# Kernel tuning notes

Hardware: AMD Instinct MI355X
Metric: run time of the kernel (lower is better)

The kernel has to match this reference:

```python
import jax, jax.numpy as jnp
import numpy as np

H = 12       # num heads
D = 64       # head dim
EPS = 1e-5

def rms_norm(x, eps=EPS):
    var = jnp.mean(jnp.square(x), axis=-1, keepdims=True)
    return x * jax.lax.rsqrt(var + eps)

def rotate_half(x):
    x1, x2 = jnp.split(x, 2, axis=-1)
    return jnp.concatenate([-x2, x1], axis=-1)

def setup_inputs() -> dict:
    key = jax.random.key(0)
    ks = jax.random.split(key, 7)
    B, S, C = 2, 2048, 768
    inter = 2048
    hidden_states = jax.random.normal(ks[0], (B, S, C), dtype=jnp.float32)
    # RoPE tables (cos/sin over positions, standard half-duplicated freqs)
    theta = 10000.0
    inv_freq = 1.0 / (theta ** (jnp.arange(0, D, 2, dtype=jnp.float32) / D))
    t = jnp.arange(S, dtype=jnp.float32)
    freqs = jnp.outer(t, inv_freq)            # [S, D/2]
    emb = jnp.concatenate([freqs, freqs], -1)  # [S, D]
    cos = jnp.cos(emb)
    sin = jnp.sin(emb)
    s = 0.02
    w_qkv = jax.random.normal(ks[1], (3 * H * D, C), dtype=jnp.float32) * s
    w_o = jax.random.normal(ks[2], (C, H * D), dtype=jnp.float32) * s
    w_gate_up = jax.random.normal(ks[3], (2 * inter, C), dtype=jnp.float32) * s
    w_down = jax.random.normal(ks[4], (C, inter), dtype=jnp.float32) * s
    return {"hidden_states": hidden_states, "cos": cos, "sin": sin,
            "w_qkv": w_qkv, "w_o": w_o, "w_gate_up": w_gate_up, "w_down": w_down}

def reference(hidden_states, cos, sin, w_qkv, w_o, w_gate_up, w_down):
    B, S, C = hidden_states.shape
    scale = 1.0 / jnp.sqrt(jnp.asarray(D, hidden_states.dtype))
    # ----- attention (manual, non-flash) -----
    qkv = jnp.einsum('bsc,ec->bse', hidden_states, w_qkv)
    qkv = qkv.reshape(B, S, 3 * H, D)
    q, k, v = qkv[:, :, :H], qkv[:, :, H:2 * H], qkv[:, :, 2 * H:]
    c = cos[None, :, None, :]
    sn = sin[None, :, None, :]
    q = q * c + rotate_half(q) * sn
    k = k * c + rotate_half(k) * sn
    scores = jnp.einsum('bihd,bjhd->bhij', q, k) * scale  # [B,H,S,S]
    attn = jax.nn.softmax(scores, axis=-1)
    ctx = jnp.einsum('bhij,bjhd->bihd', attn, v).reshape(B, S, H * D)
    attn_out = jnp.einsum('bse,ce->bsc', ctx, w_o)
    x = rms_norm(hidden_states + attn_out)
    # ----- SwiGLU MLP -----
    gu = jnp.einsum('bsc,ec->bse', x, w_gate_up)
    gate, up = jnp.split(gu, 2, axis=-1)
    mlp_out = jnp.einsum('bsi,ci->bsc', jax.nn.silu(gate) * up, w_down)
    return rms_norm(x + mlp_out)
```

## Files before the change

kernel.cpp:

```cpp
#include <hip/hip_runtime.h>


typedef __attribute__((ext_vector_type(8))) __bf16 bf16x8;
typedef __attribute__((ext_vector_type(8))) short short8;
typedef __attribute__((ext_vector_type(4))) short short4v;
typedef __attribute__((ext_vector_type(4))) float f32x4;
typedef __attribute__((ext_vector_type(4))) float float4v;
typedef __attribute__((ext_vector_type(4))) unsigned int u32x4;

#define CDIM   768
#define HEADS  12
#define DH     64
#define SEQ    2048
#define BATCH  2
#define MROWS  4096
#define QKV_N  2304
#define INTER  2048
#define GU_N   4096
#define NSPLIT 4
#define KCHUNK (SEQ / NSPLIT)
#define BH     (BATCH * HEADS)

#define QSCALE 0.18033688011112043f

static __device__ __forceinline__ unsigned short f2bf(float f) {
  unsigned int u = __builtin_bit_cast(unsigned int, f);
  u += 0x7fffu + ((u >> 16) & 1u);
  return (unsigned short)(u >> 16);
}
static __device__ __forceinline__ float bf2f(unsigned short u) {
  return __builtin_bit_cast(float, ((unsigned int)u) << 16);
}

static __device__ __forceinline__ bf16x8 ld8(const unsigned short* p) {
  return __builtin_bit_cast(bf16x8, *reinterpret_cast<const short8*>(p));
}

static __device__ __forceinline__ unsigned pack2bf(float lo, float hi) {
  unsigned short a = __builtin_bit_cast(unsigned short, (__bf16)lo);
  unsigned short b = __builtin_bit_cast(unsigned short, (__bf16)hi);
  return (unsigned)a | ((unsigned)b << 16);
}

static __device__ __forceinline__ void pl32swap(unsigned& a, unsigned& b) {
  auto r = __builtin_amdgcn_permlane32_swap(a, b, false, false);
  a = r[0]; b = r[1];
}
static __device__ __forceinline__ void pl16swap(unsigned& a, unsigned& b) {
  auto r = __builtin_amdgcn_permlane16_swap(a, b, false, false);
  a = r[0]; b = r[1];
}
static __device__ __forceinline__ float red32max(float x) {
  unsigned xi = __builtin_bit_cast(unsigned, x);
  auto r = __builtin_amdgcn_permlane32_swap(xi, xi, false, false);
  return fmaxf(__builtin_bit_cast(float, r[0]), __builtin_bit_cast(float, r[1]));
}
static __device__ __forceinline__ float red16max(float x) {
  unsigned xi = __builtin_bit_cast(unsigned, x);
  auto r = __builtin_amdgcn_permlane16_swap(xi, xi, false, false);
  return fmaxf(__builtin_bit_cast(float, r[0]), __builtin_bit_cast(float, r[1]));
}
static __device__ __forceinline__ float red32sum(float x) {
  unsigned xi = __builtin_bit_cast(unsigned, x);
  auto r = __builtin_amdgcn_permlane32_swap(xi, xi, false, false);
  return __builtin_bit_cast(float, r[0]) + __builtin_bit_cast(float, r[1]);
}
static __device__ __forceinline__ float red16sum(float x) {
  unsigned xi = __builtin_bit_cast(unsigned, x);
  auto r = __builtin_amdgcn_permlane16_swap(xi, xi, false, false);
  return __builtin_bit_cast(float, r[0]) + __builtin_bit_cast(float, r[1]);
}

__global__ __launch_bounds__(256) void cast_all(
    const float* __restrict__ h, const float* __restrict__ wqkv,
    const float* __restrict__ wo, const float* __restrict__ wgu,
    const float* __restrict__ wd,
    unsigned short* __restrict__ hb, unsigned short* __restrict__ wqkvb,
    unsigned short* __restrict__ wob, unsigned short* __restrict__ wgub,
    unsigned short* __restrict__ wdb) {
  const int n0 = 786432, n1 = 442368, n2 = 147456, n3 = 786432, n4 = 393216;
  const int total = n0 + n1 + n2 + n3 + n4;
  for (int i = blockIdx.x * blockDim.x + threadIdx.x; i < total;
       i += gridDim.x * blockDim.x) {
    int j = i;
    const float* src; unsigned short* dst;
    if      (j < n0)            { src = h;    dst = hb;    }
    else if ((j -= n0) < n1)    { src = wqkv; dst = wqkvb; }
    else if ((j -= n1) < n2)    { src = wo;   dst = wob;   }
    else if ((j -= n2) < n3)    { src = wgu;  dst = wgub;  }
    else    { j -= n3;            src = wd;   dst = wdb;   }
    float4v v = *reinterpret_cast<const float4v*>(src + 4 * (size_t)j);
    short4v o;
#pragma unroll
    for (int e = 0; e < 4; ++e) o[e] = (short)f2bf(v[e]);
    *reinterpret_cast<short4v*>(dst + 4 * (size_t)j) = o;
  }
}

template <bool BF16OUT>
__global__ __launch_bounds__(256) void gemm_lds(
    const unsigned short* __restrict__ A, const unsigned short* __restrict__ W,
    void* __restrict__ Cout, int Mm, int Nn, int Kk) {
  __shared__ unsigned short Alds[4096];
  __shared__ unsigned short Blds[4096];
  const int t = threadIdx.x;
  const int lane = t & 63, w = t >> 6;
  const int lr = lane & 15, lg = lane >> 4;
  const int row0 = blockIdx.y * 128, col0 = blockIdx.x * 128;
  const int wr = w >> 1, wc = w & 1;

  const unsigned short* ga = A + (size_t)(row0 + (t >> 2)) * Kk + (t & 3) * 8;
  const unsigned short* gb = W + (size_t)(col0 + (t >> 2)) * Kk + (t & 3) * 8;
  const size_t g64 = (size_t)64 * Kk;
  unsigned short* la0 = Alds + w * 512;
  unsigned short* lb0 = Blds + w * 512;
  const unsigned short* ra = Alds + (wr * 64 + lr) * 32 + lg * 8;
  const unsigned short* rb = Blds + (wc * 64 + lr) * 32 + lg * 8;

  f32x4 acc[4][4] = {};
  for (int k0 = 0; k0 < Kk; k0 += 32) {
    __builtin_amdgcn_global_load_lds((const unsigned int*)(ga + k0),
                                     (unsigned int*)la0, 16, 0, 0);
    __builtin_amdgcn_global_load_lds((const unsigned int*)(ga + k0 + g64),
                                     (unsigned int*)(la0 + 2048), 16, 0, 0);
    __builtin_amdgcn_global_load_lds((const unsigned int*)(gb + k0),
                                     (unsigned int*)lb0, 16, 0, 0);
    __builtin_amdgcn_global_load_lds((const unsigned int*)(gb + k0 + g64),
                                     (unsigned int*)(lb0 + 2048), 16, 0, 0);
    __syncthreads();
    bf16x8 af[4], bfr[4];
#pragma unroll
    for (int m = 0; m < 4; ++m) af[m] = ld8(ra + m * 512);
#pragma unroll
    for (int n = 0; n < 4; ++n) bfr[n] = ld8(rb + n * 512);
    __builtin_amdgcn_s_setprio(1);
#pragma unroll
    for (int m = 0; m < 4; ++m)
#pragma unroll
      for (int n = 0; n < 4; ++n)
        acc[m][n] = __builtin_amdgcn_mfma_f32_16x16x32_bf16(af[m], bfr[n],
                                                            acc[m][n], 0, 0, 0);
    __builtin_amdgcn_s_setprio(0);
    __syncthreads();
  }
#pragma unroll
  for (int m = 0; m < 4; ++m)
#pragma unroll
    for (int j = 0; j < 4; ++j) {
      const size_t roff = (size_t)(row0 + wr * 64 + m * 16 + lg * 4 + j) * Nn +
                          col0 + wc * 64 + lr;
      if constexpr (BF16OUT) {
        unsigned short* cr = (unsigned short*)Cout + roff;
#pragma unroll
        for (int n = 0; n < 4; ++n) cr[n * 16] = f2bf(acc[m][n][j]);
      } else {
        float* cr = (float*)Cout + roff;
#pragma unroll
        for (int n = 0; n < 4; ++n) cr[n * 16] = acc[m][n][j];
      }
    }
}

__global__ __launch_bounds__(256) void rope_qk(
    const unsigned short* __restrict__ qkv, const float* __restrict__ cosT,
    const float* __restrict__ sinT, unsigned short* __restrict__ qtile,
    unsigned short* __restrict__ ktile) {
  const int row = blockIdx.x * 4 + (threadIdx.x >> 6);
  const int d = threadIdx.x & 63;
  const int hh = row % 24;
  const int bs = row / 24;
  const int s = bs & (SEQ - 1);
  const int b = bs >> 11;
  float v = bf2f(qkv[(size_t)bs * QKV_N + hh * 64 + d]);
  float partner = __shfl_xor(v, 32, 64);
  float rot = (d < 32) ? -partner : partner;
  v = v * cosT[s * 64 + d] + rot * sinT[s * 64 + d];
  const int t = s >> 4, lr = s & 15;
  const int dh = d >> 5, lg = (d & 31) >> 3, j = d & 7;
  if (hh < 12) {
    const int bh = b * HEADS + hh;
    qtile[((size_t)(bh * 128 + t) * 2 + dh) * 512 + (lg * 16 + lr) * 8 + j] =
        f2bf(v * QSCALE);
  } else {
    const int bh = b * HEADS + (hh - 12);
    ktile[((size_t)(bh * 128 + t) * 2 + dh) * 512 + (lg * 16 + lr) * 8 + j] =
        f2bf(v);
  }
}

__global__ __launch_bounds__(256) void v_trans(
    const unsigned short* __restrict__ qkv, unsigned short* __restrict__ vT) {
  __shared__ unsigned short tile[64][66];
  const int bh = blockIdx.x;
  const int s0 = blockIdx.y * 64;
  const int b = bh / HEADS, h = bh % HEADS;
  const unsigned short* src = qkv + ((size_t)(b * SEQ + s0)) * QKV_N + (24 + h) * 64;
  const int d = threadIdx.x & 63, sg = threadIdx.x >> 6;
#pragma unroll
  for (int i = 0; i < 16; ++i) {
    int s = sg * 16 + i;
    tile[s][d] = src[(size_t)s * QKV_N + d];
  }
  __syncthreads();
  const int lane = threadIdx.x & 63, wid = threadIdx.x >> 6;
  const int lr = lane & 15, lg = lane >> 4;
  unsigned short* dst = vT + ((size_t)bh * 64 + (s0 >> 5)) * 4 * 512;
#pragma unroll
  for (int tt = 0; tt < 2; ++tt) {
    const int ti = wid * 2 + tt;
    const int kt = ti >> 2, d0 = (ti & 3) * 16;
    short8 o;
#pragma unroll
    for (int j = 0; j < 8; ++j)
      o[j] = (short)tile[kt * 32 + lg * 8 + j][d0 + lr];
    *reinterpret_cast<short8*>(dst + ((size_t)kt * 4 + (ti & 3)) * 512 +
                               lane * 8) = o;
  }
}

__global__ __launch_bounds__(256) void attn_fused(
    const unsigned short* __restrict__ qtile, const unsigned short* __restrict__ ktile,
    const unsigned short* __restrict__ vtile, unsigned short* __restrict__ ctxp,
    float2* __restrict__ ml) {
  const int lane = threadIdx.x & 63, wid = threadIdx.x >> 6;
  const int tid = blockIdx.x * 4 + wid;
  const int sp = tid & 3;
  const int qt = (tid >> 2) & 127;
  const int bh = tid >> 9;
  const int lr = lane & 15, lg = lane >> 4;

  const unsigned short* qp =
      qtile + ((size_t)(bh * 128 + qt) * 2) * 512 + lane * 8;
  bf16x8 qf0 = ld8(qp);
  bf16x8 qf1 = ld8(qp + 512);
  const unsigned short* kb = ktile + (size_t)bh * 128 * 2 * 512 + lane * 8;
  const unsigned short* vb = vtile + (size_t)bh * 64 * 4 * 512 + lane * 8;

  f32x4 acc0 = {0,0,0,0}, acc1 = {0,0,0,0}, acc2 = {0,0,0,0}, acc3 = {0,0,0,0};
  float m = -1e30f, l = 0.f;

  for (int k0 = sp * KCHUNK; k0 < sp * KCHUNK + KCHUNK; k0 += 32) {
    const unsigned short* kp = kb + (size_t)(k0 >> 4) * 1024;
    f32x4 st0 = {0,0,0,0}, st1 = {0,0,0,0};
    __builtin_amdgcn_s_setprio(1);
    st0 = __builtin_amdgcn_mfma_f32_16x16x32_bf16(ld8(kp),        qf0, st0, 0,0,0);
    st0 = __builtin_amdgcn_mfma_f32_16x16x32_bf16(ld8(kp + 512),  qf1, st0, 0,0,0);
    st1 = __builtin_amdgcn_mfma_f32_16x16x32_bf16(ld8(kp + 1024), qf0, st1, 0,0,0);
    st1 = __builtin_amdgcn_mfma_f32_16x16x32_bf16(ld8(kp + 1536), qf1, st1, 0,0,0);
    __builtin_amdgcn_s_setprio(0);

    float tmax = fmaxf(fmaxf(fmaxf(st0[0], st0[1]), fmaxf(st0[2], st0[3])),
                       fmaxf(fmaxf(st1[0], st1[1]), fmaxf(st1[2], st1[3])));
    tmax = red16max(red32max(tmax));

    if (tmax > m + 11.0f) {
      float fac = exp2f(m - tmax);
      m = tmax;
      l *= fac;
      acc0 *= fac; acc1 *= fac; acc2 *= fac; acc3 *= fac;
    }

    float pa[4], pb[4];
#pragma unroll
    for (int r = 0; r < 4; ++r) {
      pa[r] = exp2f(st0[r] - m);
      pb[r] = exp2f(st1[r] - m);
    }
    float ls = ((pa[0] + pa[1]) + (pa[2] + pa[3])) +
               ((pb[0] + pb[1]) + (pb[2] + pb[3]));
    l += red16sum(red32sum(ls));

    unsigned c0 = pack2bf(pa[0], pa[1]);
    unsigned c1 = pack2bf(pa[2], pa[3]);
    unsigned c2 = pack2bf(pb[0], pb[1]);
    unsigned c3 = pack2bf(pb[2], pb[3]);
    pl32swap(c0, c2);
    pl32swap(c1, c3);
    pl16swap(c0, c2);
    pl16swap(c1, c3);
    u32x4 pw = {c0, c1, c2, c3};
    bf16x8 pf = __builtin_bit_cast(bf16x8, pw);

    const unsigned short* vp = vb + (size_t)(k0 >> 5) * 2048;
    __builtin_amdgcn_s_setprio(1);
    acc0 = __builtin_amdgcn_mfma_f32_16x16x32_bf16(ld8(vp),        pf, acc0, 0,0,0);
    acc1 = __builtin_amdgcn_mfma_f32_16x16x32_bf16(ld8(vp + 512),  pf, acc1, 0,0,0);
    acc2 = __builtin_amdgcn_mfma_f32_16x16x32_bf16(ld8(vp + 1024), pf, acc2, 0,0,0);
    acc3 = __builtin_amdgcn_mfma_f32_16x16x32_bf16(ld8(vp + 1536), pf, acc3, 0,0,0);
    __builtin_amdgcn_s_setprio(0);
  }

  unsigned short* pp = ctxp +
      (((size_t)(sp * BH + bh)) * SEQ + qt * 16 + lr) * DH + 4 * lg;
  short4v o0, o1, o2, o3;
#pragma unroll
  for (int r = 0; r < 4; ++r) {
    o0[r] = (short)f2bf(acc0[r]);
    o1[r] = (short)f2bf(acc1[r]);
    o2[r] = (short)f2bf(acc2[r]);
    o3[r] = (short)f2bf(acc3[r]);
  }
  *reinterpret_cast<short4v*>(pp)      = o0;
  *reinterpret_cast<short4v*>(pp + 16) = o1;
  *reinterpret_cast<short4v*>(pp + 32) = o2;
  *reinterpret_cast<short4v*>(pp + 48) = o3;
  if (lane < 16) {
    float2 v; v.x = m; v.y = l;
    ml[(size_t)sp * (BH * SEQ) + bh * SEQ + qt * 16 + lr] = v;
  }
}

__global__ __launch_bounds__(256) void attn_combine(
    const unsigned short* __restrict__ ctxp, const float2* __restrict__ ml,
    unsigned short* __restrict__ ctx) {
  const int idx = blockIdx.x * 256 + threadIdx.x;
  const int d = idx & 63;
  const int row = idx >> 6;
  float m0 = ml[row].x,                 l0 = ml[row].y;
  float m1 = ml[row + BH*SEQ].x,        l1 = ml[row + BH*SEQ].y;
  float m2 = ml[row + 2*BH*SEQ].x,      l2 = ml[row + 2*BH*SEQ].y;
  float m3 = ml[row + 3*BH*SEQ].x,      l3 = ml[row + 3*BH*SEQ].y;
  float M = fmaxf(fmaxf(m0, m1), fmaxf(m2, m3));
  float w0 = exp2f(m0 - M), w1 = exp2f(m1 - M);
  float w2 = exp2f(m2 - M), w3 = exp2f(m3 - M);
  float den = w0 * l0 + w1 * l1 + w2 * l2 + w3 * l3;
  const size_t pstride = (size_t)BH * SEQ * DH;
  float num = w0 * bf2f(ctxp[(size_t)row * DH + d]) +
              w1 * bf2f(ctxp[(size_t)row * DH + d + pstride]) +
              w2 * bf2f(ctxp[(size_t)row * DH + d + 2 * pstride]) +
              w3 * bf2f(ctxp[(size_t)row * DH + d + 3 * pstride]);
  const int bh = row >> 11, s = row & (SEQ - 1);
  const int b = bh / HEADS, h = bh % HEADS;
  ctx[((size_t)(b * SEQ + s)) * CDIM + h * DH + d] = f2bf(num / den);
}

__global__ __launch_bounds__(256) void add_rmsnorm(
    const float* __restrict__ a, const float* __restrict__ b,
    float* __restrict__ outf, unsigned short* __restrict__ outb) {
  const int row = blockIdx.x;
  const int tid = threadIdx.x;
  const float* ap = a + (size_t)row * CDIM;
  const float* bp = b + (size_t)row * CDIM;
  float v0 = ap[tid]       + bp[tid];
  float v1 = ap[tid + 256] + bp[tid + 256];
  float v2 = ap[tid + 512] + bp[tid + 512];
  float ss = v0 * v0 + v1 * v1 + v2 * v2;
#pragma unroll
  for (int off = 32; off > 0; off >>= 1) ss += __shfl_xor(ss, off, 64);
  __shared__ float red[4];
  if ((tid & 63) == 0) red[tid >> 6] = ss;
  __syncthreads();
  float tot = red[0] + red[1] + red[2] + red[3];
  float r = rsqrtf(tot * (1.f / 768.f) + 1e-5f);
  float* of = outf + (size_t)row * CDIM;
  of[tid]       = v0 * r;
  of[tid + 256] = v1 * r;
  of[tid + 512] = v2 * r;
  if (outb) {
    unsigned short* ob = outb + (size_t)row * CDIM;
    ob[tid]       = f2bf(v0 * r);
    ob[tid + 256] = f2bf(v1 * r);
    ob[tid + 512] = f2bf(v2 * r);
  }
}

__global__ __launch_bounds__(256) void silu_mul(
    const unsigned short* __restrict__ gu, unsigned short* __restrict__ hb) {
  const int i = blockIdx.x * 256 + threadIdx.x;
  const int s = i >> 11, c = i & (INTER - 1);
  float g = bf2f(gu[(size_t)s * GU_N + c]);
  float u = bf2f(gu[(size_t)s * GU_N + INTER + c]);
  float sig = 1.f / (1.f + __expf(-g));
  hb[i] = f2bf(g * sig * u);
}

extern "C" void kernel_launch(void* const* d_in, const int* in_sizes, int n_in,
                              void* d_out, int out_size, void* d_ws, size_t ws_size,
                              hipStream_t stream) {
  const float* hidden = (const float*)d_in[0];
  const float* cosT   = (const float*)d_in[1];
  const float* sinT   = (const float*)d_in[2];
  const float* wqkv   = (const float*)d_in[3];
  const float* wo     = (const float*)d_in[4];
  const float* wgu    = (const float*)d_in[5];
  const float* wd     = (const float*)d_in[6];
  float* out = (float*)d_out;

  char* wsp = (char*)d_ws;
  size_t off = 0;
  auto alloc = [&](size_t bytes) { void* p = wsp + off; off += bytes; return p; };

  unsigned short* wqkvb = (unsigned short*)alloc(2ull * 1769472);
  unsigned short* wob   = (unsigned short*)alloc(2ull * 589824);
  unsigned short* wgub  = (unsigned short*)alloc(2ull * 3145728);
  unsigned short* wdb   = (unsigned short*)alloc(2ull * 1572864);
  unsigned short* hb    = (unsigned short*)alloc(2ull * 3145728);
  float*          x     = (float*)alloc(4ull * 3145728);
  unsigned short* xb    = (unsigned short*)alloc(2ull * 3145728);
  const size_t roff = off;

  unsigned short* qkvb = (unsigned short*)alloc(2ull * MROWS * QKV_N);
  unsigned short* qT   = (unsigned short*)alloc(2ull * MROWS * CDIM);
  unsigned short* kT   = (unsigned short*)alloc(2ull * MROWS * CDIM);
  unsigned short* vTb  = (unsigned short*)alloc(2ull * MROWS * CDIM);
  unsigned short* ctx  = (unsigned short*)alloc(2ull * MROWS * CDIM);
  float*          attn = (float*)alloc(4ull * MROWS * CDIM);
  unsigned short* ctxp = (unsigned short*)alloc(2ull * NSPLIT * BH * SEQ * DH);
  float2*         ml   = (float2*)alloc(8ull * NSPLIT * BH * SEQ);

  off = roff;
  unsigned short* gub  = (unsigned short*)alloc(2ull * MROWS * GU_N);
  unsigned short* hmid = (unsigned short*)alloc(2ull * MROWS * INTER);
  float*          mlp  = (float*)alloc(4ull * MROWS * CDIM);
  (void)ws_size; (void)in_sizes; (void)n_in; (void)out_size;

  cast_all<<<2048, 256, 0, stream>>>(hidden, wqkv, wo, wgu, wd,
                                     hb, wqkvb, wob, wgub, wdb);
  gemm_lds<true><<<dim3(QKV_N / 128, MROWS / 128), 256, 0, stream>>>(
      hb, wqkvb, qkvb, MROWS, QKV_N, CDIM);
  rope_qk<<<(MROWS * 24) / 4, 256, 0, stream>>>(qkvb, cosT, sinT, qT, kT);
  v_trans<<<dim3(BH, SEQ / 64), 256, 0, stream>>>(qkvb, vTb);
  attn_fused<<<(BH * (SEQ / 16) * NSPLIT) / 4, 256, 0, stream>>>(
      qT, kT, vTb, ctxp, ml);
  attn_combine<<<(BH * SEQ * DH) / 256, 256, 0, stream>>>(ctxp, ml, ctx);
  gemm_lds<false><<<dim3(CDIM / 128, MROWS / 128), 256, 0, stream>>>(
      ctx, wob, attn, MROWS, CDIM, CDIM);
  add_rmsnorm<<<MROWS, 256, 0, stream>>>(hidden, attn, x, xb);
  gemm_lds<true><<<dim3(GU_N / 128, MROWS / 128), 256, 0, stream>>>(
      xb, wgub, gub, MROWS, GU_N, CDIM);
  silu_mul<<<(MROWS * INTER) / 256, 256, 0, stream>>>(gub, hmid);
  gemm_lds<false><<<dim3(CDIM / 128, MROWS / 128), 256, 0, stream>>>(
      hmid, wdb, mlp, MROWS, CDIM, INTER);
  add_rmsnorm<<<MROWS, 256, 0, stream>>>(x, mlp, out, nullptr);
}
```

Before: 363.4 us.

## Use narrow GEMM tiles for small-N projections and widen attention inner step

```diff
diff --git a/kernel.cpp b/kernel.cpp
--- a/kernel.cpp
+++ b/kernel.cpp
@@ -36,10 +36,13 @@
   return __builtin_bit_cast(bf16x8, *reinterpret_cast<const short8*>(p));
 }
 
-static __device__ __forceinline__ unsigned pack2bf(float lo, float hi) {
-  unsigned short a = __builtin_bit_cast(unsigned short, (__bf16)lo);
-  unsigned short b = __builtin_bit_cast(unsigned short, (__bf16)hi);
-  return (unsigned)a | ((unsigned)b << 16);
+static __device__ __forceinline__ float exp2_raw(float x) {
+  float r; asm("v_exp_f32 %0, %1" : "=v"(r) : "v"(x)); return r;
+}
+static __device__ __forceinline__ unsigned cvtpk(float lo, float hi) {
+  unsigned r;
+  asm("v_cvt_pk_bf16_f32 %0, %1, %2" : "=v"(r) : "v"(lo), "v"(hi));
+  return r;
 }
 
 static __device__ __forceinline__ void pl32swap(unsigned& a, unsigned& b) {
@@ -97,27 +100,29 @@
   }
 }
 
-template <bool BF16OUT>
+template <int BN, bool BF16OUT>
 __global__ __launch_bounds__(256) void gemm_lds(
     const unsigned short* __restrict__ A, const unsigned short* __restrict__ W,
     void* __restrict__ Cout, int Mm, int Nn, int Kk) {
+  constexpr int MR = (BN == 128) ? 4 : 2;
   __shared__ unsigned short Alds[4096];
-  __shared__ unsigned short Blds[4096];
+  __shared__ unsigned short Blds[BN * 32];
   const int t = threadIdx.x;
   const int lane = t & 63, w = t >> 6;
   const int lr = lane & 15, lg = lane >> 4;
-  const int row0 = blockIdx.y * 128, col0 = blockIdx.x * 128;
-  const int wr = w >> 1, wc = w & 1;
+  const int row0 = blockIdx.y * 128, col0 = blockIdx.x * BN;
+  const int wrb = (BN == 128) ? (w >> 1) * 64 : w * 32;
+  const int wcb = (BN == 128) ? (w & 1) * 64 : 0;
 
   const unsigned short* ga = A + (size_t)(row0 + (t >> 2)) * Kk + (t & 3) * 8;
   const unsigned short* gb = W + (size_t)(col0 + (t >> 2)) * Kk + (t & 3) * 8;
   const size_t g64 = (size_t)64 * Kk;
   unsigned short* la0 = Alds + w * 512;
   unsigned short* lb0 = Blds + w * 512;
-  const unsigned short* ra = Alds + (wr * 64 + lr) * 32 + lg * 8;
-  const unsigned short* rb = Blds + (wc * 64 + lr) * 32 + lg * 8;
-
-  f32x4 acc[4][4] = {};
+  const unsigned short* ra = Alds + (wrb + lr) * 32 + lg * 8;
+  const unsigned short* rb = Blds + (wcb + lr) * 32 + lg * 8;
+
+  f32x4 acc[MR][4] = {};
   for (int k0 = 0; k0 < Kk; k0 += 32) {
     __builtin_amdgcn_global_load_lds((const unsigned int*)(ga + k0),
                                      (unsigned int*)la0, 16, 0, 0);
@@ -125,17 +130,18 @@
                                      (unsigned int*)(la0 + 2048), 16, 0, 0);
     __builtin_amdgcn_global_load_lds((const unsigned int*)(gb + k0),
                                      (unsigned int*)lb0, 16, 0, 0);
-    __builtin_amdgcn_global_load_lds((const unsigned int*)(gb + k0 + g64),
-                                     (unsigned int*)(lb0 + 2048), 16, 0, 0);
+    if constexpr (BN == 128)
+      __builtin_amdgcn_global_load_lds((const unsigned int*)(gb + k0 + g64),
+                                       (unsigned int*)(lb0 + 2048), 16, 0, 0);
     __syncthreads();
-    bf16x8 af[4], bfr[4];
-#pragma unroll
-    for (int m = 0; m < 4; ++m) af[m] = ld8(ra + m * 512);
+    bf16x8 af[MR], bfr[4];
+#pragma unroll
+    for (int m = 0; m < MR; ++m) af[m] = ld8(ra + m * 512);
 #pragma unroll
     for (int n = 0; n < 4; ++n) bfr[n] = ld8(rb + n * 512);
     __builtin_amdgcn_s_setprio(1);
 #pragma unroll
-    for (int m = 0; m < 4; ++m)
+    for (int m = 0; m < MR; ++m)
 #pragma unroll
       for (int n = 0; n < 4; ++n)
         acc[m][n] = __builtin_amdgcn_mfma_f32_16x16x32_bf16(af[m], bfr[n],
@@ -144,11 +150,11 @@
     __syncthreads();
   }
 #pragma unroll
-  for (int m = 0; m < 4; ++m)
+  for (int m = 0; m < MR; ++m)
 #pragma unroll
     for (int j = 0; j < 4; ++j) {
-      const size_t roff = (size_t)(row0 + wr * 64 + m * 16 + lg * 4 + j) * Nn +
-                          col0 + wc * 64 + lr;
+      const size_t roff = (size_t)(row0 + wrb + m * 16 + lg * 4 + j) * Nn +
+                          col0 + wcb + lr;
       if constexpr (BF16OUT) {
         unsigned short* cr = (unsigned short*)Cout + roff;
 #pragma unroll
@@ -237,58 +243,74 @@
   const unsigned short* vb = vtile + (size_t)bh * 64 * 4 * 512 + lane * 8;
 
   f32x4 acc0 = {0,0,0,0}, acc1 = {0,0,0,0}, acc2 = {0,0,0,0}, acc3 = {0,0,0,0};
-  float m = -1e30f, l = 0.f;
-
-  for (int k0 = sp * KCHUNK; k0 < sp * KCHUNK + KCHUNK; k0 += 32) {
+  float m = -1e30f, l_lane = 0.f;
+
+  for (int k0 = sp * KCHUNK; k0 < sp * KCHUNK + KCHUNK; k0 += 64) {
     const unsigned short* kp = kb + (size_t)(k0 >> 4) * 1024;
-    f32x4 st0 = {0,0,0,0}, st1 = {0,0,0,0};
+    f32x4 st0 = {0,0,0,0}, st1 = {0,0,0,0}, st2 = {0,0,0,0}, st3 = {0,0,0,0};
     __builtin_amdgcn_s_setprio(1);
     st0 = __builtin_amdgcn_mfma_f32_16x16x32_bf16(ld8(kp),        qf0, st0, 0,0,0);
     st0 = __builtin_amdgcn_mfma_f32_16x16x32_bf16(ld8(kp + 512),  qf1, st0, 0,0,0);
     st1 = __builtin_amdgcn_mfma_f32_16x16x32_bf16(ld8(kp + 1024), qf0, st1, 0,0,0);
     st1 = __builtin_amdgcn_mfma_f32_16x16x32_bf16(ld8(kp + 1536), qf1, st1, 0,0,0);
+    st2 = __builtin_amdgcn_mfma_f32_16x16x32_bf16(ld8(kp + 2048), qf0, st2, 0,0,0);
+    st2 = __builtin_amdgcn_mfma_f32_16x16x32_bf16(ld8(kp + 2560), qf1, st2, 0,0,0);
+    st3 = __builtin_amdgcn_mfma_f32_16x16x32_bf16(ld8(kp + 3072), qf0, st3, 0,0,0);
+    st3 = __builtin_amdgcn_mfma_f32_16x16x32_bf16(ld8(kp + 3584), qf1, st3, 0,0,0);
     __builtin_amdgcn_s_setprio(0);
 
-    float tmax = fmaxf(fmaxf(fmaxf(st0[0], st0[1]), fmaxf(st0[2], st0[3])),
-                       fmaxf(fmaxf(st1[0], st1[1]), fmaxf(st1[2], st1[3])));
+    float tmax = fmaxf(
+        fmaxf(fmaxf(fmaxf(st0[0], st0[1]), fmaxf(st0[2], st0[3])),
+              fmaxf(fmaxf(st1[0], st1[1]), fmaxf(st1[2], st1[3]))),
+        fmaxf(fmaxf(fmaxf(st2[0], st2[1]), fmaxf(st2[2], st2[3])),
+              fmaxf(fmaxf(st3[0], st3[1]), fmaxf(st3[2], st3[3]))));
     tmax = red16max(red32max(tmax));
 
     if (tmax > m + 11.0f) {
-      float fac = exp2f(m - tmax);
+      float fac = exp2_raw(m - tmax);
       m = tmax;
-      l *= fac;
+      l_lane *= fac;
       acc0 *= fac; acc1 *= fac; acc2 *= fac; acc3 *= fac;
     }
 
-    float pa[4], pb[4];
+    float p[16];
 #pragma unroll
     for (int r = 0; r < 4; ++r) {
-      pa[r] = exp2f(st0[r] - m);
-      pb[r] = exp2f(st1[r] - m);
+      p[r]      = exp2_raw(st0[r] - m);
+      p[4 + r]  = exp2_raw(st1[r] - m);
+      p[8 + r]  = exp2_raw(st2[r] - m);
+      p[12 + r] = exp2_raw(st3[r] - m);
     }
-    float ls = ((pa[0] + pa[1]) + (pa[2] + pa[3])) +
-               ((pb[0] + pb[1]) + (pb[2] + pb[3]));
-    l += red16sum(red32sum(ls));
-
-    unsigned c0 = pack2bf(pa[0], pa[1]);
-    unsigned c1 = pack2bf(pa[2], pa[3]);
-    unsigned c2 = pack2bf(pb[0], pb[1]);
-    unsigned c3 = pack2bf(pb[2], pb[3]);
-    pl32swap(c0, c2);
-    pl32swap(c1, c3);
-    pl16swap(c0, c2);
-    pl16swap(c1, c3);
-    u32x4 pw = {c0, c1, c2, c3};
-    bf16x8 pf = __builtin_bit_cast(bf16x8, pw);
+    l_lane += (((p[0] + p[1]) + (p[2] + p[3])) +
+               ((p[4] + p[5]) + (p[6] + p[7]))) +
+              (((p[8] + p[9]) + (p[10] + p[11])) +
+               ((p[12] + p[13]) + (p[14] + p[15])));
+
+    unsigned c0 = cvtpk(p[0], p[1]),   c1 = cvtpk(p[2], p[3]);
+    unsigned c2 = cvtpk(p[4], p[5]),   c3 = cvtpk(p[6], p[7]);
+    unsigned c4 = cvtpk(p[8], p[9]),   c5 = cvtpk(p[10], p[11]);
+    unsigned c6 = cvtpk(p[12], p[13]), c7 = cvtpk(p[14], p[15]);
+    pl32swap(c0, c2); pl32swap(c1, c3); pl16swap(c0, c2); pl16swap(c1, c3);
+    pl32swap(c4, c6); pl32swap(c5, c7); pl16swap(c4, c6); pl16swap(c5, c7);
+    u32x4 pw0 = {c0, c1, c2, c3};
+    u32x4 pw1 = {c4, c5, c6, c7};
+    bf16x8 pf0 = __builtin_bit_cast(bf16x8, pw0);
+    bf16x8 pf1 = __builtin_bit_cast(bf16x8, pw1);
 
     const unsigned short* vp = vb + (size_t)(k0 >> 5) * 2048;
     __builtin_amdgcn_s_setprio(1);
-    acc0 = __builtin_amdgcn_mfma_f32_16x16x32_bf16(ld8(vp),        pf, acc0, 0,0,0);
-    acc1 = __builtin_amdgcn_mfma_f32_16x16x32_bf16(ld8(vp + 512),  pf, acc1, 0,0,0);
-    acc2 = __builtin_amdgcn_mfma_f32_16x16x32_bf16(ld8(vp + 1024), pf, acc2, 0,0,0);
-    acc3 = __builtin_amdgcn_mfma_f32_16x16x32_bf16(ld8(vp + 1536), pf, acc3, 0,0,0);
+    acc0 = __builtin_amdgcn_mfma_f32_16x16x32_bf16(ld8(vp),        pf0, acc0, 0,0,0);
+    acc1 = __builtin_amdgcn_mfma_f32_16x16x32_bf16(ld8(vp + 512),  pf0, acc1, 0,0,0);
+    acc2 = __builtin_amdgcn_mfma_f32_16x16x32_bf16(ld8(vp + 1024), pf0, acc2, 0,0,0);
+    acc3 = __builtin_amdgcn_mfma_f32_16x16x32_bf16(ld8(vp + 1536), pf0, acc3, 0,0,0);
+    acc0 = __builtin_amdgcn_mfma_f32_16x16x32_bf16(ld8(vp + 2048), pf1, acc0, 0,0,0);
+    acc1 = __builtin_amdgcn_mfma_f32_16x16x32_bf16(ld8(vp + 2560), pf1, acc1, 0,0,0);
+    acc2 = __builtin_amdgcn_mfma_f32_16x16x32_bf16(ld8(vp + 3072), pf1, acc2, 0,0,0);
+    acc3 = __builtin_amdgcn_mfma_f32_16x16x32_bf16(ld8(vp + 3584), pf1, acc3, 0,0,0);
     __builtin_amdgcn_s_setprio(0);
   }
+
+  const float l = red16sum(red32sum(l_lane));
 
   unsigned short* pp = ctxp +
       (((size_t)(sp * BH + bh)) * SEQ + qt * 16 + lr) * DH + 4 * lg;
@@ -321,8 +343,8 @@
   float m2 = ml[row + 2*BH*SEQ].x,      l2 = ml[row + 2*BH*SEQ].y;
   float m3 = ml[row + 3*BH*SEQ].x,      l3 = ml[row + 3*BH*SEQ].y;
   float M = fmaxf(fmaxf(m0, m1), fmaxf(m2, m3));
-  float w0 = exp2f(m0 - M), w1 = exp2f(m1 - M);
-  float w2 = exp2f(m2 - M), w3 = exp2f(m3 - M);
+  float w0 = exp2_raw(m0 - M), w1 = exp2_raw(m1 - M);
+  float w2 = exp2_raw(m2 - M), w3 = exp2_raw(m3 - M);
   float den = w0 * l0 + w1 * l1 + w2 * l2 + w3 * l3;
   const size_t pstride = (size_t)BH * SEQ * DH;
   float num = w0 * bf2f(ctxp[(size_t)row * DH + d]) +
@@ -416,20 +438,20 @@
 
   cast_all<<<2048, 256, 0, stream>>>(hidden, wqkv, wo, wgu, wd,
                                      hb, wqkvb, wob, wgub, wdb);
-  gemm_lds<true><<<dim3(QKV_N / 128, MROWS / 128), 256, 0, stream>>>(
+  gemm_lds<128, true><<<dim3(QKV_N / 128, MROWS / 128), 256, 0, stream>>>(
       hb, wqkvb, qkvb, MROWS, QKV_N, CDIM);
   rope_qk<<<(MROWS * 24) / 4, 256, 0, stream>>>(qkvb, cosT, sinT, qT, kT);
   v_trans<<<dim3(BH, SEQ / 64), 256, 0, stream>>>(qkvb, vTb);
   attn_fused<<<(BH * (SEQ / 16) * NSPLIT) / 4, 256, 0, stream>>>(
       qT, kT, vTb, ctxp, ml);
   attn_combine<<<(BH * SEQ * DH) / 256, 256, 0, stream>>>(ctxp, ml, ctx);
-  gemm_lds<false><<<dim3(CDIM / 128, MROWS / 128), 256, 0, stream>>>(
+  gemm_lds<64, false><<<dim3(CDIM / 64, MROWS / 128), 256, 0, stream>>>(
       ctx, wob, attn, MROWS, CDIM, CDIM);
   add_rmsnorm<<<MROWS, 256, 0, stream>>>(hidden, attn, x, xb);
-  gemm_lds<true><<<dim3(GU_N / 128, MROWS / 128), 256, 0, stream>>>(
+  gemm_lds<128, true><<<dim3(GU_N / 128, MROWS / 128), 256, 0, stream>>>(
       xb, wgub, gub, MROWS, GU_N, CDIM);
   silu_mul<<<(MROWS * INTER) / 256, 256, 0, stream>>>(gub, hmid);
-  gemm_lds<false><<<dim3(CDIM / 128, MROWS / 128), 256, 0, stream>>>(
+  gemm_lds<64, false><<<dim3(CDIM / 64, MROWS / 128), 256, 0, stream>>>(
       hmid, wdb, mlp, MROWS, CDIM, INTER);
   add_rmsnorm<<<MROWS, 256, 0, stream>>>(x, mlp, out, nullptr);
 }
```

Measured after the change: 349.4 us. 1.04x faster.
